# Performance work log

Measured on AMD Instinct MI355X. Metric: run time of the kernel, lower is better.

Reference implementation:

```python
import jax, jax.numpy as jnp
import numpy as np

BS, C, D, HW = 2, 64, 64, 96
HID = 4          # hidden_rnn
R = 16           # SE reduction


def _lstm_layer(x, w_ih, w_hh, b_ih, b_hh):
    # x: [B, T, In] -> outputs [B, T, H]; PyTorch gate order (i, f, g, o)
    b = b_ih + b_hh
    Hd = w_hh.shape[1]
    B = x.shape[0]

    def step(carry, xt):
        h, c = carry
        g = xt @ w_ih.T + h @ w_hh.T + b          # [B, 4H]
        i, f, gg, o = jnp.split(g, 4, axis=-1)
        c = jax.nn.sigmoid(f) * c + jax.nn.sigmoid(i) * jnp.tanh(gg)
        h = jax.nn.sigmoid(o) * jnp.tanh(c)
        return (h, c), h

    h0 = jnp.zeros((B, Hd), x.dtype)
    (_, _), ys = jax.lax.scan(step, (h0, h0), jnp.swapaxes(x, 0, 1))
    return jnp.swapaxes(ys, 0, 1)


def _bilstm(x, layers):
    # layers: list of (wih_f, whh_f, bih_f, bhh_f, wih_b, whh_b, bih_b, bhh_b)
    y = x
    for (wif, whf, bif, bhf, wib, whb, bib, bhb) in layers:
        fwd = _lstm_layer(y, wif, whf, bif, bhf)
        bwd = _lstm_layer(y[:, ::-1], wib, whb, bib, bhb)[:, ::-1]
        y = jnp.concatenate([fwd, bwd], axis=-1)
    return y


def setup_inputs() -> dict:
    key = jax.random.key(0)
    ks = iter(jax.random.split(key, 32))
    k = 1.0 / np.sqrt(HID)
    u = lambda shp: jax.random.uniform(next(ks), shp, jnp.float32, -k, k)

    inp = {"x": jax.random.normal(next(ks), (BS, C, D, HW, HW), jnp.float32)}
    # layer 0 input size 1, layer 1 input size 2*HID
    for li, isz in ((0, 1), (1, 2 * HID)):
        for dr in ("f", "b"):
            inp[f"wih{li}{dr}"] = u((4 * HID, isz))
            inp[f"whh{li}{dr}"] = u((4 * HID, HID))
            inp[f"bih{li}{dr}"] = u((4 * HID,))
            inp[f"bhh{li}{dr}"] = u((4 * HID,))
    feat = 2 * HID * C          # 512
    inp["w1"] = jax.random.normal(next(ks), (feat // R, feat), jnp.float32) / np.sqrt(feat)
    inp["w2"] = jax.random.normal(next(ks), (C, feat // R), jnp.float32) / np.sqrt(feat // R)
    return inp


def reference(x, wih0f, whh0f, bih0f, bhh0f, wih0b, whh0b, bih0b, bhh0b,
              wih1f, whh1f, bih1f, bhh1f, wih1b, whh1b, bih1b, bhh1b, w1, w2):
    bs, c, d = x.shape[:3]
    # squeeze: adaptive avg pool over H, W -> [bs*c, d, 1]
    y = x.mean(axis=(3, 4)).reshape(bs * c, d, 1)
    layers = [(wih0f, whh0f, bih0f, bhh0f, wih0b, whh0b, bih0b, bhh0b),
              (wih1f, whh1f, bih1f, bhh1f, wih1b, whh1b, bih1b, bhh1b)]
    y = _bilstm(y, layers)                 # [bs*c, d, 2*HID]
    y = y[:, -1, :].reshape(bs, -1)        # [bs, 2*HID*c]
    y = jax.nn.sigmoid(jax.nn.relu(y @ w1.T) @ w2.T)   # [bs, c]
    return x * y[:, :, None, None, None]
```

## Files before the change

### kernel.cpp

```cpp
#include <hip/hip_runtime.h>
#include <hip/hip_bf16.h>

#define NSEQ   128
#define SEQLEN 64
#define HWHW   9216
#define CHELEM 589824

__device__ __forceinline__ float sigm(float x) {
    return 1.0f / (1.0f + __expf(-x));
}
__device__ __forceinline__ float tanhfast(float x) {
    x = fmaxf(x, -44.0f);
    float e = __expf(-2.0f * x);
    return (1.0f - e) / (1.0f + e);
}

__global__ __launch_bounds__(256) void mean_kernel(const float* __restrict__ x,
                                                   float* __restrict__ means) {
    const int bidx = blockIdx.x;
    const float4* xp = (const float4*)(x + (size_t)bidx * HWHW);
    const int tid = threadIdx.x;
    float sum = 0.f;
#pragma unroll
    for (int i = 0; i < 9; ++i) {
        float4 v = xp[tid + i * 256];
        sum += v.x + v.y + v.z + v.w;
    }
#pragma unroll
    for (int off = 32; off; off >>= 1) sum += __shfl_down(sum, off, 64);
    __shared__ float wsum[4];
    const int wave = tid >> 6, lane = tid & 63;
    if (lane == 0) wsum[wave] = sum;
    __syncthreads();
    if (tid == 0)
        means[bidx] = (wsum[0] + wsum[1] + wsum[2] + wsum[3]) * (1.0f / 9216.0f);
}

__global__ __launch_bounds__(256) void lstm_fc_kernel(
    const float* __restrict__ means,
    const float* __restrict__ wih0f, const float* __restrict__ whh0f,
    const float* __restrict__ bih0f, const float* __restrict__ bhh0f,
    const float* __restrict__ wih0b, const float* __restrict__ whh0b,
    const float* __restrict__ bih0b, const float* __restrict__ bhh0b,
    const float* __restrict__ wih1f, const float* __restrict__ whh1f,
    const float* __restrict__ bih1f, const float* __restrict__ bhh1f,
    const float* __restrict__ wih1b, const float* __restrict__ whh1b,
    const float* __restrict__ bih1b, const float* __restrict__ bhh1b,
    const float* __restrict__ w1,    const float* __restrict__ w2,
    float* __restrict__ l0out,
    float* __restrict__ scl)
{
    const int tid  = threadIdx.x;
    const int s    = tid >> 1;
    const int half = tid & 1;

    __shared__ float lastout[NSEQ][8];
    __shared__ float hidden[64];

    {
        const float* wih = half ? wih0b : wih0f;
        const float* whh = half ? whh0b : whh0f;
        const float* bi  = half ? bih0b : bih0f;
        const float* bh  = half ? bhh0b : bhh0f;
        float Wx[16], B[16], Wh[16][4];
#pragma unroll
        for (int g = 0; g < 16; ++g) {
            Wx[g] = wih[g];
            B[g]  = bi[g] + bh[g];
#pragma unroll
            for (int j = 0; j < 4; ++j) Wh[g][j] = whh[g * 4 + j];
        }
        float h[4] = {0, 0, 0, 0}, c[4] = {0, 0, 0, 0};
        const float* seq = means + s * SEQLEN;
        float xnext = seq[half ? (SEQLEN - 1) : 0];
        for (int t = 0; t < SEQLEN; ++t) {
            const int tt = half ? (SEQLEN - 1 - t) : t;
            const float xt = xnext;
            if (t < SEQLEN - 1) xnext = seq[half ? (SEQLEN - 2 - t) : (t + 1)];
            float g[16];
#pragma unroll
            for (int gi = 0; gi < 16; ++gi)
                g[gi] = fmaf(Wx[gi], xt, B[gi]) + Wh[gi][0] * h[0] + Wh[gi][1] * h[1]
                      + Wh[gi][2] * h[2] + Wh[gi][3] * h[3];
#pragma unroll
            for (int j = 0; j < 4; ++j) {
                c[j] = sigm(g[4 + j]) * c[j] + sigm(g[j]) * tanhfast(g[8 + j]);
                h[j] = sigm(g[12 + j]) * tanhfast(c[j]);
            }
            *(float4*)(l0out + (s * SEQLEN + tt) * 8 + half * 4) =
                make_float4(h[0], h[1], h[2], h[3]);
        }
    }
    __threadfence_block();
    __syncthreads();

    {
        const float* wihr = wih1f + half * 8 * 8;
        const float* whhr = whh1f + half * 8 * 4;
        const float* bir  = bih1f + half * 8;
        const float* bhr  = bhh1f + half * 8;
        float Wx[8][8], Wh[8][4], B[8];
#pragma unroll
        for (int g = 0; g < 8; ++g) {
            B[g] = bir[g] + bhr[g];
#pragma unroll
            for (int k = 0; k < 8; ++k) Wx[g][k] = wihr[g * 8 + k];
#pragma unroll
            for (int j = 0; j < 4; ++j) Wh[g][j] = whhr[g * 4 + j];
        }
        float h[4] = {0, 0, 0, 0}, c[4] = {0, 0, 0, 0};
        const float* base = l0out + s * SEQLEN * 8;
        float4 inA = *(const float4*)(base);
        float4 inB = *(const float4*)(base + 4);
        for (int t = 0; t < SEQLEN; ++t) {
            const float in[8] = {inA.x, inA.y, inA.z, inA.w, inB.x, inB.y, inB.z, inB.w};
            if (t < SEQLEN - 1) {
                inA = *(const float4*)(base + (t + 1) * 8);
                inB = *(const float4*)(base + (t + 1) * 8 + 4);
            }
            float g[8];
#pragma unroll
            for (int gi = 0; gi < 8; ++gi) {
                float acc = B[gi];
#pragma unroll
                for (int k = 0; k < 8; ++k) acc = fmaf(Wx[gi][k], in[k], acc);
#pragma unroll
                for (int j = 0; j < 4; ++j) acc = fmaf(Wh[gi][j], h[j], acc);
                g[gi] = acc;
            }
            float a[4], bg[4];
#pragma unroll
            for (int j = 0; j < 4; ++j) {
                a[j]  = half ? tanhfast(g[j]) : sigm(g[j]);
                bg[j] = sigm(g[4 + j]);
            }
#pragma unroll
            for (int j = 0; j < 4; ++j) {
                const float tg = __shfl_xor(a[j], 1);
                c[j] = bg[j] * c[j] + a[j] * tg;
                const float tc  = tanhfast(c[j]);
                const float tcx = __shfl_xor(tc, 1);
                const float hnew = bg[j] * tcx;
                const float hx   = __shfl_xor(hnew, 1);
                h[j] = half ? hnew : hx;
            }
        }
        if (!half) {
            lastout[s][0] = h[0]; lastout[s][1] = h[1];
            lastout[s][2] = h[2]; lastout[s][3] = h[3];
        }
    }

    {
        const float* wihr = wih1b + half * 8 * 8;
        const float* bir  = bih1b + half * 8;
        const float* bhr  = bhh1b + half * 8;
        const float* base = l0out + (s * SEQLEN + SEQLEN - 1) * 8;
        float4 inA = *(const float4*)(base);
        float4 inB = *(const float4*)(base + 4);
        const float in[8] = {inA.x, inA.y, inA.z, inA.w, inB.x, inB.y, inB.z, inB.w};
        float g[8];
#pragma unroll
        for (int gi = 0; gi < 8; ++gi) {
            float acc = bir[gi] + bhr[gi];
#pragma unroll
            for (int k = 0; k < 8; ++k) acc = fmaf(wihr[gi * 8 + k], in[k], acc);
            g[gi] = acc;
        }
        float a[4], bg[4];
#pragma unroll
        for (int j = 0; j < 4; ++j) {
            a[j]  = half ? tanhfast(g[j]) : sigm(g[j]);
            bg[j] = sigm(g[4 + j]);
        }
#pragma unroll
        for (int j = 0; j < 4; ++j) {
            const float tg   = __shfl_xor(a[j], 1);
            const float cnew = a[j] * tg;
            const float tc   = tanhfast(cnew);
            const float tcx  = __shfl_xor(tc, 1);
            const float hnew = bg[j] * tcx;
            if (half) lastout[s][4 + j] = hnew;
        }
    }
    __syncthreads();

    {
        const float* lastflat = &lastout[0][0];
        const int wave = tid >> 6, lane = tid & 63;
#pragma unroll
        for (int r = 0; r < 16; ++r) {
            const int o = wave * 16 + r;
            const int b = o >> 5, m = o & 31;
            float p = 0.f;
#pragma unroll
            for (int i = 0; i < 8; ++i) {
                const int k = lane + i * 64;
                p = fmaf(lastflat[b * 512 + k], w1[m * 512 + k], p);
            }
#pragma unroll
            for (int off = 32; off; off >>= 1) p += __shfl_down(p, off, 64);
            if (lane == 0) hidden[b * 32 + m] = fmaxf(p, 0.f);
        }
    }
    __syncthreads();

    if (tid < 128) {
        const int b = tid >> 6, cc = tid & 63;
        float p = 0.f;
#pragma unroll
        for (int m = 0; m < 32; ++m)
            p = fmaf(hidden[b * 32 + m], w2[cc * 32 + m], p);
        scl[tid] = sigm(p);
    }
}

__global__ __launch_bounds__(256) void scale_kernel(const float* __restrict__ x,
                                                    const float* __restrict__ scl,
                                                    float* __restrict__ out) {
    const int ch = blockIdx.y;
    const float sv = scl[ch];
    const size_t base = (size_t)ch * CHELEM + (size_t)blockIdx.x * 4096;
    const float4* xp = (const float4*)(x + base);
    float4* op = (float4*)(out + base);
    const int tid = threadIdx.x;
#pragma unroll
    for (int i = 0; i < 4; ++i) {
        float4 v = xp[tid + i * 256];
        v.x *= sv; v.y *= sv; v.z *= sv; v.w *= sv;
        op[tid + i * 256] = v;
    }
}

extern "C" void kernel_launch(void* const* d_in, const int* in_sizes, int n_in,
                              void* d_out, int out_size, void* d_ws, size_t ws_size,
                              hipStream_t stream) {
    const float* x     = (const float*)d_in[0];
    const float* wih0f = (const float*)d_in[1];
    const float* whh0f = (const float*)d_in[2];
    const float* bih0f = (const float*)d_in[3];
    const float* bhh0f = (const float*)d_in[4];
    const float* wih0b = (const float*)d_in[5];
    const float* whh0b = (const float*)d_in[6];
    const float* bih0b = (const float*)d_in[7];
    const float* bhh0b = (const float*)d_in[8];
    const float* wih1f = (const float*)d_in[9];
    const float* whh1f = (const float*)d_in[10];
    const float* bih1f = (const float*)d_in[11];
    const float* bhh1f = (const float*)d_in[12];
    const float* wih1b = (const float*)d_in[13];
    const float* whh1b = (const float*)d_in[14];
    const float* bih1b = (const float*)d_in[15];
    const float* bhh1b = (const float*)d_in[16];
    const float* w1    = (const float*)d_in[17];
    const float* w2    = (const float*)d_in[18];
    float* out = (float*)d_out;

    float* ws    = (float*)d_ws;
    float* means = ws;
    float* l0out = ws + 8192;
    float* scl   = ws + 8192 + 65536;

    mean_kernel<<<dim3(8192), dim3(256), 0, stream>>>(x, means);
    lstm_fc_kernel<<<dim3(1), dim3(256), 0, stream>>>(
        means,
        wih0f, whh0f, bih0f, bhh0f, wih0b, whh0b, bih0b, bhh0b,
        wih1f, whh1f, bih1f, bhh1f, wih1b, whh1b, bih1b, bhh1b,
        w1, w2, l0out, scl);
    scale_kernel<<<dim3(144, 128), dim3(256), 0, stream>>>(x, scl, out);
}
```

Baseline: 697.3 us.

## Reverse scale traversal for cache reuse, nontemporal stores, and shorten LSTM shuffle chain

The scale kernel now walks channels and chunks in reverse order, so the tail of x that mean_kernel read last may still sit in the large last-level cache when it is read again. Its output stores become nontemporal so they do not evict that data. The LSTM cell update exchanges gate activations once with two parallel shuffles instead of three dependent ones, which shortens the serial recurrence on the single-block critical path. The reverse mapping depends on how blocks are actually dispatched, and the reworked lane role selection has to reproduce the original gate pairing exactly.

```diff
diff --git a/kernel.cpp b/kernel.cpp
--- a/kernel.cpp
+++ b/kernel.cpp
@@ -5,6 +5,9 @@
 #define SEQLEN 64
 #define HWHW   9216
 #define CHELEM 589824
+#define NCHUNK 144
+
+typedef float v4f __attribute__((ext_vector_type(4)));
 
 __device__ __forceinline__ float sigm(float x) {
     return 1.0f / (1.0f + __expf(-x));
@@ -18,13 +21,13 @@
 __global__ __launch_bounds__(256) void mean_kernel(const float* __restrict__ x,
                                                    float* __restrict__ means) {
     const int bidx = blockIdx.x;
-    const float4* xp = (const float4*)(x + (size_t)bidx * HWHW);
+    const v4f* xp = (const v4f*)(x + (size_t)bidx * HWHW);
     const int tid = threadIdx.x;
     float sum = 0.f;
 #pragma unroll
     for (int i = 0; i < 9; ++i) {
-        float4 v = xp[tid + i * 256];
-        sum += v.x + v.y + v.z + v.w;
+        v4f v = xp[tid + i * 256];
+        sum += v[0] + v[1] + v[2] + v[3];
     }
 #pragma unroll
     for (int off = 32; off; off >>= 1) sum += __shfl_down(sum, off, 64);
@@ -136,13 +139,14 @@
             }
 #pragma unroll
             for (int j = 0; j < 4; ++j) {
-                const float tg = __shfl_xor(a[j], 1);
-                c[j] = bg[j] * c[j] + a[j] * tg;
-                const float tc  = tanhfast(c[j]);
-                const float tcx = __shfl_xor(tc, 1);
-                const float hnew = bg[j] * tcx;
-                const float hx   = __shfl_xor(hnew, 1);
-                h[j] = half ? hnew : hx;
+                const float ax = __shfl_xor(a[j], 1);
+                const float bx = __shfl_xor(bg[j], 1);
+                const float si = half ? ax    : a[j];
+                const float sf = half ? bx    : bg[j];
+                const float tg = half ? a[j]  : ax;
+                const float so = half ? bg[j] : bx;
+                c[j] = fmaf(sf, c[j], si * tg);
+                h[j] = so * tanhfast(c[j]);
             }
         }
         if (!half) {
@@ -175,12 +179,14 @@
         }
 #pragma unroll
         for (int j = 0; j < 4; ++j) {
-            const float tg   = __shfl_xor(a[j], 1);
-            const float cnew = a[j] * tg;
-            const float tc   = tanhfast(cnew);
-            const float tcx  = __shfl_xor(tc, 1);
-            const float hnew = bg[j] * tcx;
-            if (half) lastout[s][4 + j] = hnew;
+            const float ax = __shfl_xor(a[j], 1);
+            const float bx = __shfl_xor(bg[j], 1);
+            const float si = half ? ax    : a[j];
+            const float tg = half ? a[j]  : ax;
+            const float so = half ? bg[j] : bx;
+            const float cnew = si * tg;
+            const float hnew = so * tanhfast(cnew);
+            if (!half) lastout[s][4 + j] = hnew;
         }
     }
     __syncthreads();
@@ -218,17 +224,18 @@
 __global__ __launch_bounds__(256) void scale_kernel(const float* __restrict__ x,
                                                     const float* __restrict__ scl,
                                                     float* __restrict__ out) {
-    const int ch = blockIdx.y;
+    const int ch    = 127 - blockIdx.y;
+    const int chunk = (NCHUNK - 1) - blockIdx.x;
     const float sv = scl[ch];
-    const size_t base = (size_t)ch * CHELEM + (size_t)blockIdx.x * 4096;
-    const float4* xp = (const float4*)(x + base);
-    float4* op = (float4*)(out + base);
+    const size_t base = (size_t)ch * CHELEM + (size_t)chunk * 4096;
+    const v4f* xp = (const v4f*)(x + base);
+    v4f* op = (v4f*)(out + base);
     const int tid = threadIdx.x;
 #pragma unroll
     for (int i = 0; i < 4; ++i) {
-        float4 v = xp[tid + i * 256];
-        v.x *= sv; v.y *= sv; v.z *= sv; v.w *= sv;
-        op[tid + i * 256] = v;
+        v4f v = xp[tid + i * 256];
+        v *= sv;
+        __builtin_nontemporal_store(v, op + tid + i * 256);
     }
 }
 
@@ -267,5 +274,5 @@
         wih0f, whh0f, bih0f, bhh0f, wih0b, whh0b, bih0b, bhh0b,
         wih1f, whh1f, bih1f, bhh1f, wih1b, whh1b, bih1b, bhh1b,
         w1, w2, l0out, scl);
-    scale_kernel<<<dim3(144, 128), dim3(256), 0, stream>>>(x, scl, out);
-}
+    scale_kernel<<<dim3(NCHUNK, 128), dim3(256), 0, stream>>>(x, scl, out);
+}
```

After: 684.3 us. No clear change (-1.9%).
